# Optimization experiments

Measured on AMD Instinct MI355X. Metric: run time of the kernel, lower is better.

The kernel has to match this reference:

```python
import jax, jax.numpy as jnp
import numpy as np

P = 10      # num_prototypes == embed_dim
H = 2       # num_heads
F = 64      # ffn_dim
L = 2       # transformer_blocks
DH = P // H # head dim = 5


def _layernorm(x, g, b, eps=1e-5):
    mu = jnp.mean(x, axis=-1, keepdims=True)
    var = jnp.var(x, axis=-1, keepdims=True)
    return (x - mu) * jax.lax.rsqrt(var + eps) * g + b


def setup_inputs() -> dict:
    key = jax.random.key(0)
    ks = jax.random.split(key, 16)
    B = 1_000_000
    inp = {
        "x": jax.random.normal(ks[0], (B, 8), dtype=jnp.float32),
        "prototypes": jax.random.normal(ks[1], (P, 8), dtype=jnp.float32),
        # attention projections, stacked over layers
        "Wq": jax.random.normal(ks[2], (L, P, P), dtype=jnp.float32) * 0.1,
        "bq": jnp.zeros((L, P), dtype=jnp.float32),
        "Wk": jax.random.normal(ks[3], (L, P, P), dtype=jnp.float32) * 0.1,
        "bk": jnp.zeros((L, P), dtype=jnp.float32),
        "Wv": jax.random.normal(ks[4], (L, P, P), dtype=jnp.float32) * 0.1,
        "bv": jnp.zeros((L, P), dtype=jnp.float32),
        "Wo": jax.random.normal(ks[5], (L, P, P), dtype=jnp.float32) * 0.1,
        "bo": jnp.zeros((L, P), dtype=jnp.float32),
        "ln1_g": jnp.ones((L, P), dtype=jnp.float32),
        "ln1_b": jnp.zeros((L, P), dtype=jnp.float32),
        "ln2_g": jnp.ones((L, P), dtype=jnp.float32),
        "ln2_b": jnp.zeros((L, P), dtype=jnp.float32),
        # FFN
        "W1": jax.random.normal(ks[6], (L, P, F), dtype=jnp.float32) * 0.1,
        "b1": jnp.zeros((L, F), dtype=jnp.float32),
        "W2": jax.random.normal(ks[7], (L, F, P), dtype=jnp.float32) * 0.1,
        "b2": jnp.zeros((L, P), dtype=jnp.float32),
        # classifier (num_classes=2 -> single logit + sigmoid)
        "Wc": jax.random.normal(ks[8], (P, 1), dtype=jnp.float32) * 0.1,
        "bc": jnp.zeros((1,), dtype=jnp.float32),
    }
    return inp


def _forward(x, prototypes, Wq, bq, Wk, bk, Wv, bv, Wo, bo,
             ln1_g, ln1_b, ln2_g, ln2_b, W1, b1, W2, b2, Wc, bc):
    # ---- vectorized RBF kernel matrix (replaces the B*P python loop) ----
    x2 = jnp.sum(x * x, axis=-1, keepdims=True)            # [B,1]
    p2 = jnp.sum(prototypes * prototypes, axis=-1)          # [P]
    sq = x2 + p2[None, :] - 2.0 * (x @ prototypes.T)        # [B,P]
    km = jnp.exp(-sq)                                       # [B,P] quantum-kernel proxy

    seq = km[:, None, :]                                    # [B, S=1, P]
    scale = 1.0 / jnp.sqrt(jnp.asarray(DH, dtype=seq.dtype))
    B = seq.shape[0]

    for l in range(L):  # small fixed layer count
        # pre-norm multi-head self-attention (seq_len == 1)
        h = _layernorm(seq, ln1_g[l], ln1_b[l])
        q = (h @ Wq[l] + bq[l]).reshape(B, 1, H, DH)
        k = (h @ Wk[l] + bk[l]).reshape(B, 1, H, DH)
        v = (h @ Wv[l] + bv[l]).reshape(B, 1, H, DH)
        scores = jnp.einsum('bqhd,bkhd->bhqk', q, k) * scale
        attn = jax.nn.softmax(scores, axis=-1)
        o = jnp.einsum('bhqk,bkhd->bqhd', attn, v).reshape(B, 1, P)
        seq = seq + (o @ Wo[l] + bo[l])
        # pre-norm FFN
        h2 = _layernorm(seq, ln2_g[l], ln2_b[l])
        seq = seq + (jax.nn.gelu(h2 @ W1[l] + b1[l]) @ W2[l] + b2[l])

    logits = seq[:, 0, :] @ Wc + bc                          # [B,1]
    return jax.nn.sigmoid(logits)


def reference(x, prototypes, Wq, bq, Wk, bk, Wv, bv, Wo, bo,
              ln1_g, ln1_b, ln2_g, ln2_b, W1, b1, W2, b2, Wc, bc):
    return _forward(x, prototypes, Wq, bq, Wk, bk, Wv, bv, Wo, bo,
                    ln1_g, ln1_b, ln2_g, ln2_b, W1, b1, W2, b2, Wc, bc)
```

## Files before the change

kernel.cpp:

```cpp
#include <hip/hip_runtime.h>
#include <cmath>

#define PP 10
#define FF 64
#define LL 2
#define BLOCK 256
#define L2E 1.44269504088896f

typedef float f32x4 __attribute__((ext_vector_type(4)));
typedef _Float16 f16x4 __attribute__((ext_vector_type(4)));
typedef _Float16 h2 __attribute__((ext_vector_type(2)));

struct GeluCoef { float c[5]; };

#define FB_B1 2304
#define FB_C1 4352
#define FB_B2 4864
#define FB_WC 5120
#define F_HC  5376

__device__ __forceinline__ float fast_sigmoid(float z) {
    return __builtin_amdgcn_rcpf(1.0f + exp2f(-L2E * z));
}

__device__ __forceinline__ unsigned int pack_h2f(float a, float b) {
    _Float16 ha = (_Float16)a, hb = (_Float16)b;
    unsigned short ua = __builtin_bit_cast(unsigned short, ha);
    unsigned short ub = __builtin_bit_cast(unsigned short, hb);
    return (unsigned int)ua | ((unsigned int)ub << 16);
}

__device__ __forceinline__ h2 h2bcast(float v) {
    _Float16 h = (_Float16)v;
    h2 r; r.x = h; r.y = h; return r;
}

#define MFMA(a, b, c) __builtin_amdgcn_mfma_f32_16x16x16f16((a), (b), (c), 0, 0, 0)

__global__ __launch_bounds__(256) void prep2(
    const float* __restrict__ Wv, const float* __restrict__ bv,
    const float* __restrict__ Wo, const float* __restrict__ bo,
    const float* __restrict__ ln1g, const float* __restrict__ ln1b,
    const float* __restrict__ ln2g, const float* __restrict__ ln2b,
    const float* __restrict__ W1, const float* __restrict__ b1,
    const float* __restrict__ W2, const float* __restrict__ b2,
    const float* __restrict__ Wc, const float* __restrict__ bc,
    float* __restrict__ ws)
{
    const int t = threadIdx.x;
    unsigned int* wsu = (unsigned int*)ws;

    for (int idx = t; idx < 18 * 128; idx += 256) {
        int F = idx >> 7, d = idx & 127;
        int ln = d >> 1, half = d & 1;
        int row = ln & 15;
        int k0 = 4 * (ln >> 4) + 2 * half;
        float v[2] = {0.0f, 0.0f};
        if (F < 2) {
            int l = F;
            if (row < PP) {
                for (int kk = 0; kk < 2; ++kk) {
                    int j = k0 + kk;
                    if (j < PP) {
                        float s = 0.0f;
                        for (int m = 0; m < PP; ++m)
                            s += Wv[l*PP*PP + j*PP + m] * Wo[l*PP*PP + m*PP + row];
                        v[kk] = ln1g[l*PP + j] * s;
                    }
                }
            }
        } else if (F < 10) {
            int l = (F - 2) >> 2, m = (F - 2) & 3;
            int f = 16 * m + row;
            for (int kk = 0; kk < 2; ++kk) {
                int j = k0 + kk;
                if (j < PP) v[kk] = ln2g[l*PP + j] * W1[l*PP*FF + j*FF + f];
            }
        } else if (F < 14) {
            int c = F - 10;
            if (row < PP) {
                for (int kk = 0; kk < 2; ++kk) {
                    int f = 16 * c + k0 + kk;
                    v[kk] = W2[f*PP + row];
                }
            }
        } else {
            int c = F - 14;
            if (row == 0) {
                for (int kk = 0; kk < 2; ++kk) {
                    int f = 16 * c + k0 + kk;
                    float s = 0.0f;
                    for (int o = 0; o < PP; ++o) s += W2[FF*PP + f*PP + o] * Wc[o];
                    v[kk] = s;
                }
            }
        }
        wsu[idx] = pack_h2f(v[0], v[1]);
    }

    for (int idx = t; idx < 2048; idx += 256) {
        int lm = idx >> 8; int l = lm >> 2, m = lm & 3;
        int r2 = idx & 255; int ln = r2 >> 2, rr = r2 & 3;
        int f = 16 * m + 4 * (ln >> 4) + rr;
        float s = b1[l*FF + f];
        for (int j = 0; j < PP; ++j) s += ln2b[l*PP + j] * W1[l*PP*FF + j*FF + f];
        ws[FB_B1 + idx] = s;
    }

    for (int idx = t; idx < 512; idx += 256) {
        int l = idx >> 8;
        int r2 = idx & 255; int ln = r2 >> 2, rr = r2 & 3;
        int o = 4 * (ln >> 4) + rr;
        float val = 0.0f;
        if (o < PP) {
            float s = bo[l*PP + o];
            for (int m = 0; m < PP; ++m) s += bv[l*PP + m] * Wo[l*PP*PP + m*PP + o];
            for (int j = 0; j < PP; ++j) {
                float ww = 0.0f;
                for (int m = 0; m < PP; ++m)
                    ww += Wv[l*PP*PP + j*PP + m] * Wo[l*PP*PP + m*PP + o];
                s += ln1b[l*PP + j] * ww;
            }
            val = s;
        }
        ws[FB_C1 + idx] = val;
    }

    if (t < 256) {
        int ln = t >> 2, rr = t & 3;
        int o = 4 * (ln >> 4) + rr;
        ws[FB_B2 + t] = (o < PP) ? b2[o] : 0.0f;
        ws[FB_WC + t] = (o < PP) ? Wc[o] : 0.0f;
    }
    if (t == 0) {
        float s = bc[0];
        for (int o = 0; o < PP; ++o) s += Wc[o] * b2[PP + o];
        ws[F_HC] = s;
    }
}


__device__ __forceinline__ f16x4 ln_pack(f32x4 s) {
    float ls = (s.x + s.y) + (s.z + s.w);
    float lq = fmaf(s.x, s.x, fmaf(s.y, s.y, fmaf(s.z, s.z, s.w * s.w)));
    ls += __shfl_xor(ls, 16); ls += __shfl_xor(ls, 32);
    lq += __shfl_xor(lq, 16); lq += __shfl_xor(lq, 32);
    float mu = ls * 0.1f;
    float var = fmaf(-mu, mu, lq * 0.1f);
    float rs = __builtin_amdgcn_rsqf(var + 1e-5f);
    float mrs = -mu * rs;
    uint2 u;
    u.x = pack_h2f(fmaf(s.x, rs, mrs), fmaf(s.y, rs, mrs));
    u.y = pack_h2f(fmaf(s.z, rs, mrs), fmaf(s.w, rs, mrs));
    return __builtin_bit_cast(f16x4, u);
}

__device__ __forceinline__ f16x4 gelu_pack(f32x4 tv, h2 G0, h2 G1, h2 G2, h2 G3,
                                           h2 G4, h2 HLF) {
    h2 X0 = __builtin_bit_cast(h2, pack_h2f(tv.x, tv.y));
    h2 X1 = __builtin_bit_cast(h2, pack_h2f(tv.z, tv.w));
    h2 S0 = X0 * X0, S1 = X1 * X1;
    h2 P0 = S0 * G4 + G3, P1 = S1 * G4 + G3;
    P0 = S0 * P0 + G2; P1 = S1 * P1 + G2;
    P0 = S0 * P0 + G1; P1 = S1 * P1 + G1;
    P0 = S0 * P0 + G0; P1 = S1 * P1 + G0;
    h2 H0 = X0 * P0 + HLF, H1 = X1 * P1 + HLF;
    h2 U0 = X0 * H0, U1 = X1 * H1;
    uint2 u;
    u.x = __builtin_bit_cast(unsigned int, U0);
    u.y = __builtin_bit_cast(unsigned int, U1);
    return __builtin_bit_cast(f16x4, u);
}

__global__ __launch_bounds__(BLOCK) void hq_mfma(
    const float* __restrict__ x, const float* __restrict__ protos,
    const float* __restrict__ ws, float* __restrict__ out, int B, GeluCoef gc)
{
    const int t = threadIdx.x;
    const int lane = t & 63;
    const int q = lane >> 4;
    const int col = lane & 15;
    const int wbase = blockIdx.x * BLOCK + (t >> 6) * 64;

    const uint2* fr = (const uint2*)ws;
    f16x4 aattn[2], affn1[2][4], affn2[4], aw2c[4];
#pragma unroll
    for (int l = 0; l < 2; ++l)
        aattn[l] = __builtin_bit_cast(f16x4, fr[l * 64 + lane]);
#pragma unroll
    for (int l = 0; l < 2; ++l)
#pragma unroll
        for (int m = 0; m < 4; ++m)
            affn1[l][m] = __builtin_bit_cast(f16x4, fr[(2 + l * 4 + m) * 64 + lane]);
#pragma unroll
    for (int c = 0; c < 4; ++c)
        affn2[c] = __builtin_bit_cast(f16x4, fr[(10 + c) * 64 + lane]);
#pragma unroll
    for (int c = 0; c < 4; ++c)
        aw2c[c] = __builtin_bit_cast(f16x4, fr[(14 + c) * 64 + lane]);

    const f32x4* wv4 = (const f32x4*)ws;
    f32x4 b1f[2][4], c1f[2];
#pragma unroll
    for (int l = 0; l < 2; ++l) {
#pragma unroll
        for (int m = 0; m < 4; ++m) b1f[l][m] = wv4[576 + (l * 4 + m) * 64 + lane];
        c1f[l] = wv4[1088 + l * 64 + lane];
    }
    f32x4 b2f = wv4[1216 + lane];
    f32x4 wcf = wv4[1280 + lane];
    float hc = ws[F_HC];
    f32x4 zi = {0.0f, 0.0f, 0.0f, 0.0f};
    if (q == 0) zi.x = hc;

    const float4* p4 = (const float4*)protos;
    float mp2[4];
#pragma unroll
    for (int r = 0; r < 4; ++r) {
        int p = 4 * q + r;
        int pc = (p < PP) ? p : 0;
        float4 a = p4[pc * 2], b = p4[pc * 2 + 1];
        float s2 = a.x * a.x + a.y * a.y + a.z * a.z + a.w * a.w
                 + b.x * b.x + b.y * b.y + b.z * b.z + b.w * b.w;
        mp2[r] = (p < PP) ? (-L2E * s2) : -1e30f;
    }

    const float4* x4 = (const float4*)x;
    f32x4 seq[4];
#pragma unroll
    for (int g = 0; g < 4; ++g) {
        int e = wbase + g * 16 + col;
        if (e >= B) e = B - 1;
        float4 xa = x4[e * 2], xb = x4[e * 2 + 1];
        float x2 = xa.x * xa.x + xa.y * xa.y + xa.z * xa.z + xa.w * xa.w
                 + xb.x * xb.x + xb.y * xb.y + xb.z * xb.z + xb.w * xb.w;
#pragma unroll
        for (int r = 0; r < 4; ++r) {
            int p = 4 * q + r;
            int pc = (p < PP) ? p : 0;
            float4 a = p4[pc * 2], b = p4[pc * 2 + 1];
            float dot = xa.x * a.x + xa.y * a.y + xa.z * a.z + xa.w * a.w
                      + xb.x * b.x + xb.y * b.y + xb.z * b.z + xb.w * b.w;
            float s = fmaf(2.0f * L2E, dot, fmaf(-L2E, x2, mp2[r]));
            seq[g][r] = exp2f(s);
        }
    }

    const h2 GC0 = h2bcast(gc.c[0]);
    const h2 GC1 = h2bcast(gc.c[1]);
    const h2 GC2 = h2bcast(gc.c[2]);
    const h2 GC3 = h2bcast(gc.c[3]);
    const h2 GC4 = h2bcast(gc.c[4]);
    const h2 HLF = h2bcast(0.5f);

#pragma unroll
    for (int l = 0; l < 2; ++l) {
#pragma unroll
        for (int g = 0; g < 4; ++g) {
            f16x4 y = ln_pack(seq[g]);
            f32x4 d = MFMA(aattn[l], y, c1f[l]);
            seq[g] += d;
        }
        if (l == 0) {
#pragma unroll
            for (int g = 0; g < 4; ++g) {
                f16x4 y = ln_pack(seq[g]);
                f16x4 u0 = gelu_pack(MFMA(affn1[0][0], y, b1f[0][0]), GC0, GC1, GC2, GC3, GC4, HLF);
                f16x4 u1 = gelu_pack(MFMA(affn1[0][1], y, b1f[0][1]), GC0, GC1, GC2, GC3, GC4, HLF);
                f16x4 u2 = gelu_pack(MFMA(affn1[0][2], y, b1f[0][2]), GC0, GC1, GC2, GC3, GC4, HLF);
                f16x4 u3 = gelu_pack(MFMA(affn1[0][3], y, b1f[0][3]), GC0, GC1, GC2, GC3, GC4, HLF);
                f32x4 o2 = MFMA(affn2[0], u0, b2f);
                o2 = MFMA(affn2[1], u1, o2);
                o2 = MFMA(affn2[2], u2, o2);
                o2 = MFMA(affn2[3], u3, o2);
                seq[g] += o2;
            }
        } else {
#pragma unroll
            for (int g = 0; g < 4; ++g) {
                f16x4 y = ln_pack(seq[g]);
                f16x4 u0 = gelu_pack(MFMA(affn1[1][0], y, b1f[1][0]), GC0, GC1, GC2, GC3, GC4, HLF);
                f16x4 u1 = gelu_pack(MFMA(affn1[1][1], y, b1f[1][1]), GC0, GC1, GC2, GC3, GC4, HLF);
                f16x4 u2 = gelu_pack(MFMA(affn1[1][2], y, b1f[1][2]), GC0, GC1, GC2, GC3, GC4, HLF);
                f16x4 u3 = gelu_pack(MFMA(affn1[1][3], y, b1f[1][3]), GC0, GC1, GC2, GC3, GC4, HLF);
                f32x4 zc = MFMA(aw2c[0], u0, zi);
                zc = MFMA(aw2c[1], u1, zc);
                zc = MFMA(aw2c[2], u2, zc);
                zc = MFMA(aw2c[3], u3, zc);
                float wcs = fmaf(wcf.x, seq[g].x,
                            fmaf(wcf.y, seq[g].y,
                            fmaf(wcf.z, seq[g].z, wcf.w * seq[g].w)));
                wcs += __shfl_xor(wcs, 16);
                wcs += __shfl_xor(wcs, 32);
                float z = wcs + zc.x;
                float r = fast_sigmoid(z);
                if (q == 0) {
                    int e0 = wbase + g * 16 + col;
                    if (e0 < B) out[e0] = r;
                }
            }
        }
    }
}

extern "C" void kernel_launch(void* const* d_in, const int* in_sizes, int n_in,
                              void* d_out, int out_size, void* d_ws, size_t ws_size,
                              hipStream_t stream) {
    const float* x      = (const float*)d_in[0];
    const float* protos = (const float*)d_in[1];
    const float* Wv   = (const float*)d_in[6];
    const float* bv   = (const float*)d_in[7];
    const float* Wo   = (const float*)d_in[8];
    const float* bo   = (const float*)d_in[9];
    const float* ln1g = (const float*)d_in[10];
    const float* ln1b = (const float*)d_in[11];
    const float* ln2g = (const float*)d_in[12];
    const float* ln2b = (const float*)d_in[13];
    const float* W1   = (const float*)d_in[14];
    const float* b1   = (const float*)d_in[15];
    const float* W2   = (const float*)d_in[16];
    const float* b2   = (const float*)d_in[17];
    const float* Wc   = (const float*)d_in[18];
    const float* bc   = (const float*)d_in[19];
    float* out = (float*)d_out;
    float* ws  = (float*)d_ws;

    GeluCoef gcoef;
    {
        const double PI = 3.14159265358979323846;
        const double cc = 0.7978845608028654, aa = 0.044715;
        double sv[5], gd[5];
        for (int k = 0; k < 5; ++k) {
            double tk = 1.85 + 1.85 * std::cos((2 * k + 1) * PI / 10.0);
            sv[k] = tk * tk;
            gd[k] = std::tanh(cc * (tk + aa * tk * tk * tk)) / tk;
        }
        for (int j = 1; j < 5; ++j)
            for (int i = 4; i >= j; --i)
                gd[i] = (gd[i] - gd[i - 1]) / (sv[i] - sv[i - j]);
        double c[5] = {0, 0, 0, 0, 0};
        c[0] = gd[4];
        for (int k = 3; k >= 0; --k) {
            for (int i = 4; i >= 1; --i) c[i] = c[i - 1] - sv[k] * c[i];
            c[0] = -sv[k] * c[0] + gd[k];
        }
        for (int i = 0; i < 5; ++i) gcoef.c[i] = (float)(0.5 * c[i]);
    }

    prep2<<<1, 256, 0, stream>>>(Wv, bv, Wo, bo, ln1g, ln1b, ln2g, ln2b,
                                 W1, b1, W2, b2, Wc, bc, ws);

    const int B = in_sizes[0] / 8;
    const int grid = (B + BLOCK - 1) / BLOCK;
    hq_mfma<<<grid, BLOCK, 0, stream>>>(x, protos, ws, out, B, gcoef);
}
```

Before: 177.6 us.

## Fold biases into MFMA via constant-one input row and process 8 groups per wave

```diff
diff --git a/kernel.cpp b/kernel.cpp
--- a/kernel.cpp
+++ b/kernel.cpp
@@ -3,8 +3,9 @@
 
 #define PP 10
 #define FF 64
-#define LL 2
 #define BLOCK 256
+#define NG 8
+#define EPB ((BLOCK / 64) * NG * 16)
 #define L2E 1.44269504088896f
 
 typedef float f32x4 __attribute__((ext_vector_type(4)));
@@ -13,11 +14,9 @@
 
 struct GeluCoef { float c[5]; };
 
-#define FB_B1 2304
-#define FB_C1 4352
-#define FB_B2 4864
-#define FB_WC 5120
-#define F_HC  5376
+#define NFRAG 19
+#define FB_B2 (NFRAG * 128)
+#define F_HC  (FB_B2 + 256)
 
 __device__ __forceinline__ float fast_sigmoid(float z) {
     return __builtin_amdgcn_rcpf(1.0f + exp2f(-L2E * z));
@@ -50,7 +49,7 @@
     const int t = threadIdx.x;
     unsigned int* wsu = (unsigned int*)ws;
 
-    for (int idx = t; idx < 18 * 128; idx += 256) {
+    for (int idx = t; idx < NFRAG * 128; idx += 256) {
         int F = idx >> 7, d = idx & 127;
         int ln = d >> 1, half = d & 1;
         int row = ln & 15;
@@ -66,6 +65,17 @@
                         for (int m = 0; m < PP; ++m)
                             s += Wv[l*PP*PP + j*PP + m] * Wo[l*PP*PP + m*PP + row];
                         v[kk] = ln1g[l*PP + j] * s;
+                    } else if (j == PP) {
+                        float s = bo[l*PP + row];
+                        for (int m = 0; m < PP; ++m)
+                            s += bv[l*PP + m] * Wo[l*PP*PP + m*PP + row];
+                        for (int jj = 0; jj < PP; ++jj) {
+                            float ww = 0.0f;
+                            for (int m = 0; m < PP; ++m)
+                                ww += Wv[l*PP*PP + jj*PP + m] * Wo[l*PP*PP + m*PP + row];
+                            s += ln1b[l*PP + jj] * ww;
+                        }
+                        v[kk] = s;
                     }
                 }
             }
@@ -74,7 +84,14 @@
             int f = 16 * m + row;
             for (int kk = 0; kk < 2; ++kk) {
                 int j = k0 + kk;
-                if (j < PP) v[kk] = ln2g[l*PP + j] * W1[l*PP*FF + j*FF + f];
+                if (j < PP) {
+                    v[kk] = ln2g[l*PP + j] * W1[l*PP*FF + j*FF + f];
+                } else if (j == PP) {
+                    float s = b1[l*FF + f];
+                    for (int jj = 0; jj < PP; ++jj)
+                        s += ln2b[l*PP + jj] * W1[l*PP*FF + jj*FF + f];
+                    v[kk] = s;
+                }
             }
         } else if (F < 14) {
             int c = F - 10;
@@ -84,7 +101,7 @@
                     v[kk] = W2[f*PP + row];
                 }
             }
-        } else {
+        } else if (F < 18) {
             int c = F - 14;
             if (row == 0) {
                 for (int kk = 0; kk < 2; ++kk) {
@@ -94,43 +111,21 @@
                     v[kk] = s;
                 }
             }
+        } else {
+            if (row == 0) {
+                for (int kk = 0; kk < 2; ++kk) {
+                    int k = k0 + kk;
+                    if (k < PP) v[kk] = Wc[k];
+                }
+            }
         }
         wsu[idx] = pack_h2f(v[0], v[1]);
-    }
-
-    for (int idx = t; idx < 2048; idx += 256) {
-        int lm = idx >> 8; int l = lm >> 2, m = lm & 3;
-        int r2 = idx & 255; int ln = r2 >> 2, rr = r2 & 3;
-        int f = 16 * m + 4 * (ln >> 4) + rr;
-        float s = b1[l*FF + f];
-        for (int j = 0; j < PP; ++j) s += ln2b[l*PP + j] * W1[l*PP*FF + j*FF + f];
-        ws[FB_B1 + idx] = s;
-    }
-
-    for (int idx = t; idx < 512; idx += 256) {
-        int l = idx >> 8;
-        int r2 = idx & 255; int ln = r2 >> 2, rr = r2 & 3;
-        int o = 4 * (ln >> 4) + rr;
-        float val = 0.0f;
-        if (o < PP) {
-            float s = bo[l*PP + o];
-            for (int m = 0; m < PP; ++m) s += bv[l*PP + m] * Wo[l*PP*PP + m*PP + o];
-            for (int j = 0; j < PP; ++j) {
-                float ww = 0.0f;
-                for (int m = 0; m < PP; ++m)
-                    ww += Wv[l*PP*PP + j*PP + m] * Wo[l*PP*PP + m*PP + o];
-                s += ln1b[l*PP + j] * ww;
-            }
-            val = s;
-        }
-        ws[FB_C1 + idx] = val;
     }
 
     if (t < 256) {
         int ln = t >> 2, rr = t & 3;
         int o = 4 * (ln >> 4) + rr;
         ws[FB_B2 + t] = (o < PP) ? b2[o] : 0.0f;
-        ws[FB_WC + t] = (o < PP) ? Wc[o] : 0.0f;
     }
     if (t == 0) {
         float s = bc[0];
@@ -140,7 +135,7 @@
 }
 
 
-__device__ __forceinline__ f16x4 ln_pack(f32x4 s) {
+__device__ __forceinline__ f16x4 ln_pack(f32x4 s, int q) {
     float ls = (s.x + s.y) + (s.z + s.w);
     float lq = fmaf(s.x, s.x, fmaf(s.y, s.y, fmaf(s.z, s.z, s.w * s.w)));
     ls += __shfl_xor(ls, 16); ls += __shfl_xor(ls, 32);
@@ -151,7 +146,8 @@
     float mrs = -mu * rs;
     uint2 u;
     u.x = pack_h2f(fmaf(s.x, rs, mrs), fmaf(s.y, rs, mrs));
-    u.y = pack_h2f(fmaf(s.z, rs, mrs), fmaf(s.w, rs, mrs));
+    u.y = (q == 2) ? 0x00003C00u
+                   : pack_h2f(fmaf(s.z, rs, mrs), fmaf(s.w, rs, mrs));
     return __builtin_bit_cast(f16x4, u);
 }
 
@@ -172,7 +168,7 @@
     return __builtin_bit_cast(f16x4, u);
 }
 
-__global__ __launch_bounds__(BLOCK) void hq_mfma(
+__global__ __launch_bounds__(BLOCK, 2) void hq_mfma(
     const float* __restrict__ x, const float* __restrict__ protos,
     const float* __restrict__ ws, float* __restrict__ out, int B, GeluCoef gc)
 {
@@ -180,10 +176,10 @@
     const int lane = t & 63;
     const int q = lane >> 4;
     const int col = lane & 15;
-    const int wbase = blockIdx.x * BLOCK + (t >> 6) * 64;
+    const int wbase = blockIdx.x * EPB + (t >> 6) * (NG * 16);
 
     const uint2* fr = (const uint2*)ws;
-    f16x4 aattn[2], affn1[2][4], affn2[4], aw2c[4];
+    f16x4 aattn[2], affn1[2][4], affn2[4], aw2c[4], ahead;
 #pragma unroll
     for (int l = 0; l < 2; ++l)
         aattn[l] = __builtin_bit_cast(f16x4, fr[l * 64 + lane]);
@@ -198,49 +194,41 @@
 #pragma unroll
     for (int c = 0; c < 4; ++c)
         aw2c[c] = __builtin_bit_cast(f16x4, fr[(14 + c) * 64 + lane]);
+    ahead = __builtin_bit_cast(f16x4, fr[18 * 64 + lane]);
 
     const f32x4* wv4 = (const f32x4*)ws;
-    f32x4 b1f[2][4], c1f[2];
-#pragma unroll
-    for (int l = 0; l < 2; ++l) {
-#pragma unroll
-        for (int m = 0; m < 4; ++m) b1f[l][m] = wv4[576 + (l * 4 + m) * 64 + lane];
-        c1f[l] = wv4[1088 + l * 64 + lane];
-    }
-    f32x4 b2f = wv4[1216 + lane];
-    f32x4 wcf = wv4[1280 + lane];
+    f32x4 b2f = wv4[FB_B2 / 4 + lane];
     float hc = ws[F_HC];
-    f32x4 zi = {0.0f, 0.0f, 0.0f, 0.0f};
-    if (q == 0) zi.x = hc;
+    f32x4 zero4 = {0.0f, 0.0f, 0.0f, 0.0f};
+    f32x4 zi = zero4;
+    if (lane < 16) zi.x = hc;
 
     const float4* p4 = (const float4*)protos;
+    float4 pa[4], pb[4];
     float mp2[4];
 #pragma unroll
     for (int r = 0; r < 4; ++r) {
         int p = 4 * q + r;
         int pc = (p < PP) ? p : 0;
-        float4 a = p4[pc * 2], b = p4[pc * 2 + 1];
-        float s2 = a.x * a.x + a.y * a.y + a.z * a.z + a.w * a.w
-                 + b.x * b.x + b.y * b.y + b.z * b.z + b.w * b.w;
+        pa[r] = p4[pc * 2]; pb[r] = p4[pc * 2 + 1];
+        float s2 = pa[r].x*pa[r].x + pa[r].y*pa[r].y + pa[r].z*pa[r].z + pa[r].w*pa[r].w
+                 + pb[r].x*pb[r].x + pb[r].y*pb[r].y + pb[r].z*pb[r].z + pb[r].w*pb[r].w;
         mp2[r] = (p < PP) ? (-L2E * s2) : -1e30f;
     }
 
     const float4* x4 = (const float4*)x;
-    f32x4 seq[4];
-#pragma unroll
-    for (int g = 0; g < 4; ++g) {
+    f32x4 seq[NG];
+#pragma unroll
+    for (int g = 0; g < NG; ++g) {
         int e = wbase + g * 16 + col;
         if (e >= B) e = B - 1;
         float4 xa = x4[e * 2], xb = x4[e * 2 + 1];
-        float x2 = xa.x * xa.x + xa.y * xa.y + xa.z * xa.z + xa.w * xa.w
-                 + xb.x * xb.x + xb.y * xb.y + xb.z * xb.z + xb.w * xb.w;
+        float x2 = xa.x*xa.x + xa.y*xa.y + xa.z*xa.z + xa.w*xa.w
+                 + xb.x*xb.x + xb.y*xb.y + xb.z*xb.z + xb.w*xb.w;
 #pragma unroll
         for (int r = 0; r < 4; ++r) {
-            int p = 4 * q + r;
-            int pc = (p < PP) ? p : 0;
-            float4 a = p4[pc * 2], b = p4[pc * 2 + 1];
-            float dot = xa.x * a.x + xa.y * a.y + xa.z * a.z + xa.w * a.w
-                      + xb.x * b.x + xb.y * b.y + xb.z * b.z + xb.w * b.w;
+            float dot = xa.x*pa[r].x + xa.y*pa[r].y + xa.z*pa[r].z + xa.w*pa[r].w
+                      + xb.x*pb[r].x + xb.y*pb[r].y + xb.z*pb[r].z + xb.w*pb[r].w;
             float s = fmaf(2.0f * L2E, dot, fmaf(-L2E, x2, mp2[r]));
             seq[g][r] = exp2f(s);
         }
@@ -253,53 +241,58 @@
     const h2 GC4 = h2bcast(gc.c[4]);
     const h2 HLF = h2bcast(0.5f);
 
-#pragma unroll
-    for (int l = 0; l < 2; ++l) {
-#pragma unroll
-        for (int g = 0; g < 4; ++g) {
-            f16x4 y = ln_pack(seq[g]);
-            f32x4 d = MFMA(aattn[l], y, c1f[l]);
-            seq[g] += d;
-        }
-        if (l == 0) {
-#pragma unroll
-            for (int g = 0; g < 4; ++g) {
-                f16x4 y = ln_pack(seq[g]);
-                f16x4 u0 = gelu_pack(MFMA(affn1[0][0], y, b1f[0][0]), GC0, GC1, GC2, GC3, GC4, HLF);
-                f16x4 u1 = gelu_pack(MFMA(affn1[0][1], y, b1f[0][1]), GC0, GC1, GC2, GC3, GC4, HLF);
-                f16x4 u2 = gelu_pack(MFMA(affn1[0][2], y, b1f[0][2]), GC0, GC1, GC2, GC3, GC4, HLF);
-                f16x4 u3 = gelu_pack(MFMA(affn1[0][3], y, b1f[0][3]), GC0, GC1, GC2, GC3, GC4, HLF);
-                f32x4 o2 = MFMA(affn2[0], u0, b2f);
-                o2 = MFMA(affn2[1], u1, o2);
-                o2 = MFMA(affn2[2], u2, o2);
-                o2 = MFMA(affn2[3], u3, o2);
-                seq[g] += o2;
-            }
-        } else {
-#pragma unroll
-            for (int g = 0; g < 4; ++g) {
-                f16x4 y = ln_pack(seq[g]);
-                f16x4 u0 = gelu_pack(MFMA(affn1[1][0], y, b1f[1][0]), GC0, GC1, GC2, GC3, GC4, HLF);
-                f16x4 u1 = gelu_pack(MFMA(affn1[1][1], y, b1f[1][1]), GC0, GC1, GC2, GC3, GC4, HLF);
-                f16x4 u2 = gelu_pack(MFMA(affn1[1][2], y, b1f[1][2]), GC0, GC1, GC2, GC3, GC4, HLF);
-                f16x4 u3 = gelu_pack(MFMA(affn1[1][3], y, b1f[1][3]), GC0, GC1, GC2, GC3, GC4, HLF);
-                f32x4 zc = MFMA(aw2c[0], u0, zi);
-                zc = MFMA(aw2c[1], u1, zc);
-                zc = MFMA(aw2c[2], u2, zc);
-                zc = MFMA(aw2c[3], u3, zc);
-                float wcs = fmaf(wcf.x, seq[g].x,
-                            fmaf(wcf.y, seq[g].y,
-                            fmaf(wcf.z, seq[g].z, wcf.w * seq[g].w)));
-                wcs += __shfl_xor(wcs, 16);
-                wcs += __shfl_xor(wcs, 32);
-                float z = wcs + zc.x;
-                float r = fast_sigmoid(z);
-                if (q == 0) {
-                    int e0 = wbase + g * 16 + col;
-                    if (e0 < B) out[e0] = r;
-                }
-            }
-        }
+    f16x4 y[NG];
+
+#pragma unroll
+    for (int g = 0; g < NG; ++g) y[g] = ln_pack(seq[g], q);
+#pragma unroll
+    for (int g = 0; g < NG; ++g) seq[g] = MFMA(aattn[0], y[g], seq[g]);
+#pragma unroll
+    for (int g = 0; g < NG; ++g) y[g] = ln_pack(seq[g], q);
+#pragma unroll
+    for (int g = 0; g < NG; ++g) {
+        f32x4 t0 = MFMA(affn1[0][0], y[g], zero4);
+        f32x4 t1 = MFMA(affn1[0][1], y[g], zero4);
+        f32x4 t2 = MFMA(affn1[0][2], y[g], zero4);
+        f32x4 t3 = MFMA(affn1[0][3], y[g], zero4);
+        f16x4 u0 = gelu_pack(t0, GC0, GC1, GC2, GC3, GC4, HLF);
+        f16x4 u1 = gelu_pack(t1, GC0, GC1, GC2, GC3, GC4, HLF);
+        f16x4 u2 = gelu_pack(t2, GC0, GC1, GC2, GC3, GC4, HLF);
+        f16x4 u3 = gelu_pack(t3, GC0, GC1, GC2, GC3, GC4, HLF);
+        f32x4 o = MFMA(affn2[0], u0, seq[g]);
+        o = MFMA(affn2[1], u1, o);
+        o = MFMA(affn2[2], u2, o);
+        o = MFMA(affn2[3], u3, o);
+        seq[g] = o + b2f;
+    }
+
+#pragma unroll
+    for (int g = 0; g < NG; ++g) y[g] = ln_pack(seq[g], q);
+#pragma unroll
+    for (int g = 0; g < NG; ++g) seq[g] = MFMA(aattn[1], y[g], seq[g]);
+#pragma unroll
+    for (int g = 0; g < NG; ++g) y[g] = ln_pack(seq[g], q);
+#pragma unroll
+    for (int g = 0; g < NG; ++g) {
+        f32x4 t0 = MFMA(affn1[1][0], y[g], zero4);
+        f32x4 t1 = MFMA(affn1[1][1], y[g], zero4);
+        f32x4 t2 = MFMA(affn1[1][2], y[g], zero4);
+        f32x4 t3 = MFMA(affn1[1][3], y[g], zero4);
+        f16x4 u0 = gelu_pack(t0, GC0, GC1, GC2, GC3, GC4, HLF);
+        f16x4 u1 = gelu_pack(t1, GC0, GC1, GC2, GC3, GC4, HLF);
+        f16x4 u2 = gelu_pack(t2, GC0, GC1, GC2, GC3, GC4, HLF);
+        f16x4 u3 = gelu_pack(t3, GC0, GC1, GC2, GC3, GC4, HLF);
+        f32x4 zc = MFMA(aw2c[0], u0, zi);
+        zc = MFMA(aw2c[1], u1, zc);
+        zc = MFMA(aw2c[2], u2, zc);
+        zc = MFMA(aw2c[3], u3, zc);
+        uint2 sh;
+        sh.x = pack_h2f(seq[g].x, seq[g].y);
+        sh.y = pack_h2f(seq[g].z, seq[g].w);
+        zc = MFMA(ahead, __builtin_bit_cast(f16x4, sh), zc);
+        float r = fast_sigmoid(zc.x);
+        int e0 = wbase + g * 16 + col;
+        if (q == 0 && e0 < B) out[e0] = r;
     }
 }
 
@@ -351,6 +344,6 @@
                                  W1, b1, W2, b2, Wc, bc, ws);
 
     const int B = in_sizes[0] / 8;
-    const int grid = (B + BLOCK - 1) / BLOCK;
+    const int grid = (B + EPB - 1) / EPB;
     hq_mfma<<<grid, BLOCK, 0, stream>>>(x, protos, ws, out, B, gcoef);
 }
```

After: 155.3 us. 1.14x faster.
